# Kernel optimization log

Hardware: AMD Instinct MI355X
Metric: run time of the kernel (lower is better)

## Reference

```python
import jax, jax.numpy as jnp
import numpy as np

NEG_SLOPE = 0.2


def gat_layer(x, src, dst, W, a_src, a_dst, b, heads, out_c, concat):
    N = x.shape[0]
    h = (x @ W).reshape(N, heads, out_c)                      # [N,H,C]
    alpha_s = jnp.einsum('nhc,hc->nh', h, a_src)              # [N,H]
    alpha_d = jnp.einsum('nhc,hc->nh', h, a_dst)              # [N,H]
    e = jax.nn.leaky_relu(alpha_s[src] + alpha_d[dst], NEG_SLOPE)  # [E,H]
    # softmax over incoming edges per destination node (segment softmax)
    m = jax.ops.segment_max(e, dst, num_segments=N)
    m = jnp.where(jnp.isfinite(m), m, 0.0)
    ex = jnp.exp(e - m[dst])
    denom = jax.ops.segment_sum(ex, dst, num_segments=N)
    alpha = ex / (denom[dst] + 1e-16)                         # [E,H]
    out = jax.ops.segment_sum(alpha[:, :, None] * h[src], dst, num_segments=N)  # [N,H,C]
    out = out.reshape(N, heads * out_c) if concat else out.mean(axis=1)
    return out + b


def setup_inputs() -> dict:
    key = jax.random.key(0)
    ks = jax.random.split(key, 12)
    N, E, D, H, C, G = 20000, 160000, 256, 4, 128, 64
    x = jax.random.normal(ks[0], (N, D), dtype=jnp.float32)
    edge_index = jax.random.randint(ks[1], (2, E), 0, N)
    batch = jnp.sort(jax.random.randint(ks[2], (N,), 0, G))
    s = 0.05
    params = {
        'W1': jax.random.normal(ks[3], (D, H * C), jnp.float32) * s,
        'a_src1': jax.random.normal(ks[4], (H, C), jnp.float32) * s,
        'a_dst1': jax.random.normal(ks[5], (H, C), jnp.float32) * s,
        'b1': jnp.zeros((H * C,), jnp.float32),
        'W2': jax.random.normal(ks[6], (H * C, C), jnp.float32) * s,
        'a_src2': jax.random.normal(ks[7], (1, C), jnp.float32) * s,
        'a_dst2': jax.random.normal(ks[8], (1, C), jnp.float32) * s,
        'b2': jnp.zeros((C,), jnp.float32),
        'fc1_W': jax.random.normal(ks[9], (C, C // 2), jnp.float32) * s,
        'fc1_b': jnp.zeros((C // 2,), jnp.float32),
        'fc2_W': jax.random.normal(ks[10], (C // 2, 1), jnp.float32) * s,
        'fc2_b': jnp.zeros((1,), jnp.float32),
    }
    return dict(x=x, edge_index=edge_index, batch=batch, **params)


def reference(x, edge_index, batch, W1, a_src1, a_dst1, b1, W2, a_src2, a_dst2, b2,
              fc1_W, fc1_b, fc2_W, fc2_b):
    N = x.shape[0]
    G = 64  # number of graphs
    # add self-loops (PyG GATConv default)
    loop = jnp.arange(N, dtype=edge_index.dtype)
    src = jnp.concatenate([edge_index[0], loop])
    dst = jnp.concatenate([edge_index[1], loop])
    h = jax.nn.relu(gat_layer(x, src, dst, W1, a_src1, a_dst1, b1, 4, 128, True))
    h = gat_layer(h, src, dst, W2, a_src2, a_dst2, b2, 1, 128, False)
    # global mean pool per graph
    sums = jax.ops.segment_sum(h, batch, num_segments=G)
    cnts = jax.ops.segment_sum(jnp.ones((N,), h.dtype), batch, num_segments=G)
    pooled = sums / jnp.maximum(cnts, 1.0)[:, None]          # [G,128]
    out = jax.nn.relu(pooled @ fc1_W + fc1_b)
    return out @ fc2_W + fc2_b                                # [G,1]
```

## Files before the change

### kernel.cpp

```cpp
#include <hip/hip_runtime.h>
#include <hip/hip_bf16.h>
#include <cstdint>
#include <cstddef>

#define NEG_SLOPE 0.2f

typedef __attribute__((ext_vector_type(8))) __bf16 bf16x8;
typedef __attribute__((ext_vector_type(4))) __bf16 bf16x4;
typedef __attribute__((ext_vector_type(2))) __bf16 bf16x2;
typedef __attribute__((ext_vector_type(4))) float  f32x4;

template<int MF, int NF, bool STORE_BF16>
__global__ __launch_bounds__(256) void gemm_mfma(
    const __bf16* __restrict__ A, const __bf16* __restrict__ Bhi,
    const __bf16* __restrict__ Blo, void* __restrict__ Cout,
    int M, int N, int K)
{
    const int tid  = threadIdx.x;
    const int wave = tid >> 6, lane = tid & 63;
    const int wr = wave >> 1, wc = wave & 1;
    const int rowbase = blockIdx.y * (32 * MF) + wr * (16 * MF);
    const int colbase = blockIdx.x * (32 * NF) + wc * (16 * NF);
    const int l15 = lane & 15, kg = lane >> 4;

    size_t aoff[MF], boff[NF];
    #pragma unroll
    for (int mf = 0; mf < MF; ++mf) {
        int r = rowbase + mf * 16 + l15;
        if (r > M - 1) r = M - 1;
        aoff[mf] = (size_t)r * K + kg * 8;
    }
    #pragma unroll
    for (int nf = 0; nf < NF; ++nf) {
        int c = colbase + nf * 16 + l15;
        boff[nf] = (size_t)c * K + kg * 8;
    }

    f32x4 acc[MF][NF];
    #pragma unroll
    for (int mf = 0; mf < MF; ++mf)
        #pragma unroll
        for (int nf = 0; nf < NF; ++nf)
            acc[mf][nf] = (f32x4){0.f, 0.f, 0.f, 0.f};

    #pragma unroll 2
    for (int k0 = 0; k0 < K; k0 += 32) {
        bf16x8 af[MF], bh[NF], bl[NF];
        #pragma unroll
        for (int mf = 0; mf < MF; ++mf)
            af[mf] = *(const bf16x8*)(A + aoff[mf] + k0);
        #pragma unroll
        for (int nf = 0; nf < NF; ++nf) {
            bh[nf] = *(const bf16x8*)(Bhi + boff[nf] + k0);
            bl[nf] = *(const bf16x8*)(Blo + boff[nf] + k0);
        }
        #pragma unroll
        for (int mf = 0; mf < MF; ++mf)
            #pragma unroll
            for (int nf = 0; nf < NF; ++nf) {
                acc[mf][nf] = __builtin_amdgcn_mfma_f32_16x16x32_bf16(af[mf], bh[nf], acc[mf][nf], 0, 0, 0);
                acc[mf][nf] = __builtin_amdgcn_mfma_f32_16x16x32_bf16(af[mf], bl[nf], acc[mf][nf], 0, 0, 0);
            }
    }

    #pragma unroll
    for (int mf = 0; mf < MF; ++mf)
        #pragma unroll
        for (int j = 0; j < 4; ++j) {
            int r = rowbase + mf * 16 + kg * 4 + j;
            if (r < M) {
                #pragma unroll
                for (int nf = 0; nf < NF; ++nf) {
                    int c = colbase + nf * 16 + l15;
                    if (STORE_BF16)
                        ((__bf16*)Cout)[(size_t)r * N + c] = (__bf16)acc[mf][nf][j];
                    else
                        ((float*)Cout)[(size_t)r * N + c] = acc[mf][nf][j];
                }
            }
        }
}

__global__ void prep_kernel(const float* __restrict__ W1, const float* __restrict__ W2,
                            const float* __restrict__ as1w, const float* __restrict__ ad1w,
                            const float* __restrict__ as2w, const float* __restrict__ ad2w,
                            const int* __restrict__ batch,
                            __bf16* __restrict__ w1thi, __bf16* __restrict__ w1tlo,
                            __bf16* __restrict__ w2thi, __bf16* __restrict__ w2tlo,
                            float* __restrict__ wsd1, float* __restrict__ wsd2,
                            int* __restrict__ gstart, int* __restrict__ cnt,
                            int N, int G)
{
    int t = blockIdx.x * 256 + threadIdx.x;
    if (t < 131072) {
        int i = t;
        int k = i >> 9, n = i & 511;
        float w = W1[i];
        __bf16 hi = (__bf16)w;
        __bf16 lo = (__bf16)(w - (float)hi);
        w1thi[n * 256 + k] = hi;
        w1tlo[n * 256 + k] = lo;
    } else if (t < 196608) {
        int j = t - 131072;
        int k = j >> 7, n = j & 127;
        float w = W2[j];
        __bf16 hi = (__bf16)w;
        __bf16 lo = (__bf16)(w - (float)hi);
        w2thi[n * 512 + k] = hi;
        w2tlo[n * 512 + k] = lo;
    } else if (t < 199680) {
        int t2 = t - 196608;
        if (t2 < 2048) {
            int k = t2 >> 3, v = t2 & 7, h = v >> 1;
            const float* av = (v & 1) ? (ad1w + h * 128) : (as1w + h * 128);
            float s = 0.f;
            for (int c = 0; c < 128; ++c) s += W1[k * 512 + h * 128 + c] * av[c];
            wsd1[v * 256 + k] = s;
        } else {
            int t3 = t2 - 2048;
            int k = t3 >> 1, v = t3 & 1;
            const float* av = v ? ad2w : as2w;
            float s = 0.f;
            for (int c = 0; c < 128; ++c) s += W2[k * 128 + c] * av[c];
            wsd2[v * 512 + k] = s;
        }
    } else if (t < 199680 + N) {
        int n = t - 199680;
        int b    = batch[n];
        int prev = (n == 0) ? -1 : batch[n - 1];
        for (int g = prev + 1; g <= b; ++g) gstart[g] = n;
        if (n == N - 1) {
            for (int g = b + 1; g <= G; ++g) gstart[g] = N;
        }
    } else if (t < 199680 + 2 * N) {
        cnt[t - 199680 - N] = 0;
    }
}

__global__ __launch_bounds__(256) void cvtx_kernel(
    const float* __restrict__ x, const float* __restrict__ wsd1,
    __bf16* __restrict__ xb, float* __restrict__ as1_, float* __restrict__ ad1_, int N)
{
    int wave = threadIdx.x >> 6, lane = threadIdx.x & 63;
    int n = blockIdx.x * 4 + wave;
    if (n >= N) return;
    float4 xv = *(const float4*)&x[(size_t)n * 256 + lane * 4];
    bf16x4 xo;
    xo[0] = (__bf16)xv.x; xo[1] = (__bf16)xv.y; xo[2] = (__bf16)xv.z; xo[3] = (__bf16)xv.w;
    *(bf16x4*)&xb[(size_t)n * 256 + lane * 4] = xo;
    float p[8];
    #pragma unroll
    for (int v = 0; v < 8; ++v) {
        float4 wv = *(const float4*)&wsd1[v * 256 + lane * 4];
        p[v] = xv.x * wv.x + xv.y * wv.y + xv.z * wv.z + xv.w * wv.w;
    }
    #pragma unroll
    for (int v = 0; v < 8; ++v)
        #pragma unroll
        for (int s = 1; s < 64; s <<= 1) p[v] += __shfl_xor(p[v], s);
    if (lane == 0) {
        #pragma unroll
        for (int h = 0; h < 4; ++h) {
            as1_[n * 4 + h] = p[2 * h];
            ad1_[n * 4 + h] = p[2 * h + 1];
        }
    }
}

__global__ void count_kernel(const int* __restrict__ ei, int* __restrict__ cnt,
                             int ET, int E0)
{
    int e = blockIdx.x * blockDim.x + threadIdx.x;
    if (e >= ET) return;
    int d = (e < E0) ? ei[E0 + e] : (e - E0);
    atomicAdd(&cnt[d], 1);
}

__global__ void scan1(const int* __restrict__ cnt, int* __restrict__ offs,
                      int* __restrict__ bsum, int n)
{
    __shared__ int tmp[256];
    int t = threadIdx.x;
    int i = blockIdx.x * 256 + t;
    int v = (i < n) ? cnt[i] : 0;
    tmp[t] = v;
    __syncthreads();
    for (int s = 1; s < 256; s <<= 1) {
        int a = (t >= s) ? tmp[t - s] : 0;
        __syncthreads();
        tmp[t] += a;
        __syncthreads();
    }
    if (i < n) offs[i] = tmp[t] - v;
    if (t == 255) bsum[blockIdx.x] = tmp[255];
}

__global__ void scan2(const int* __restrict__ bsum, int* __restrict__ bofs,
                      int B, int* __restrict__ total_dst)
{
    __shared__ int tmp[256];
    int t = threadIdx.x;
    int v = (t < B) ? bsum[t] : 0;
    tmp[t] = v;
    __syncthreads();
    for (int s = 1; s < 256; s <<= 1) {
        int a = (t >= s) ? tmp[t - s] : 0;
        __syncthreads();
        tmp[t] += a;
        __syncthreads();
    }
    if (t < B) bofs[t] = tmp[t] - v;
    if (t == 255) *total_dst = tmp[255];
}

__global__ void scan3(int* __restrict__ offs, const int* __restrict__ bofs,
                      int* __restrict__ cur, int n)
{
    int i = blockIdx.x * 256 + threadIdx.x;
    if (i < n) {
        int o = offs[i] + bofs[blockIdx.x];
        offs[i] = o;
        cur[i]  = o;
    }
}

__global__ void scatter_kernel(const int* __restrict__ ei, int* __restrict__ cur,
                               int* __restrict__ eid, int ET, int E0)
{
    int e = blockIdx.x * blockDim.x + threadIdx.x;
    if (e >= ET) return;
    int d   = (e < E0) ? ei[E0 + e] : (e - E0);
    int pos = atomicAdd(&cur[d], 1);
    eid[pos] = e;
}

__global__ __launch_bounds__(256) void aggregate1_kernel(
    const __bf16* __restrict__ h1b, const int* __restrict__ offs,
    const int* __restrict__ eid, const int* __restrict__ ei,
    const float* __restrict__ as1_, const float* __restrict__ ad1_,
    const float* __restrict__ b1, const float* __restrict__ wsd2,
    __bf16* __restrict__ out1b, float* __restrict__ as2_, float* __restrict__ ad2_,
    int E0, int N)
{
    int wave = threadIdx.x >> 6, lane = threadIdx.x & 63;
    int n = blockIdx.x * 4 + wave;
    if (n >= N) return;
    int hd  = lane >> 4;
    int l16 = lane & 15;
    int s0 = offs[n], s1 = offs[n + 1];
    float adn = ad1_[n * 4 + hd];

    float m = -1e30f;
    for (int j = s0 + l16; j < s1; j += 16) {
        int e = eid[j];
        int s = (e < E0) ? ei[e] : (e - E0);
        float v = as1_[s * 4 + hd] + adn;
        v = (v < 0.f) ? NEG_SLOPE * v : v;
        m = fmaxf(m, v);
    }
    #pragma unroll
    for (int t = 1; t < 16; t <<= 1) m = fmaxf(m, __shfl_xor(m, t));
    float den = 0.f;
    for (int j = s0 + l16; j < s1; j += 16) {
        int e = eid[j];
        int s = (e < E0) ? ei[e] : (e - E0);
        float v = as1_[s * 4 + hd] + adn;
        v = (v < 0.f) ? NEG_SLOPE * v : v;
        den += __expf(v - m);
    }
    #pragma unroll
    for (int t = 1; t < 16; t <<= 1) den += __shfl_xor(den, t);
    float inv = 1.f / (den + 1e-16f);

    float a[8] = {0.f, 0.f, 0.f, 0.f, 0.f, 0.f, 0.f, 0.f};
    const __bf16* hbase = h1b + lane * 8;
    int j = s0;
    for (; j + 3 < s1; j += 4) {
        int e0 = eid[j], e1 = eid[j + 1], e2 = eid[j + 2], e3 = eid[j + 3];
        int sA = (e0 < E0) ? ei[e0] : (e0 - E0);
        int sB = (e1 < E0) ? ei[e1] : (e1 - E0);
        int sC = (e2 < E0) ? ei[e2] : (e2 - E0);
        int sD = (e3 < E0) ? ei[e3] : (e3 - E0);
        float vA = as1_[sA * 4 + hd] + adn;
        float vB = as1_[sB * 4 + hd] + adn;
        float vC = as1_[sC * 4 + hd] + adn;
        float vD = as1_[sD * 4 + hd] + adn;
        bf16x8 hA = *(const bf16x8*)(hbase + (size_t)sA * 512);
        bf16x8 hB = *(const bf16x8*)(hbase + (size_t)sB * 512);
        bf16x8 hC = *(const bf16x8*)(hbase + (size_t)sC * 512);
        bf16x8 hD = *(const bf16x8*)(hbase + (size_t)sD * 512);
        vA = (vA < 0.f) ? NEG_SLOPE * vA : vA;
        vB = (vB < 0.f) ? NEG_SLOPE * vB : vB;
        vC = (vC < 0.f) ? NEG_SLOPE * vC : vC;
        vD = (vD < 0.f) ? NEG_SLOPE * vD : vD;
        float wA = __expf(vA - m) * inv;
        float wB = __expf(vB - m) * inv;
        float wC = __expf(vC - m) * inv;
        float wD = __expf(vD - m) * inv;
        #pragma unroll
        for (int i = 0; i < 8; ++i) {
            a[i] = fmaf(wA, (float)hA[i], a[i]);
            a[i] = fmaf(wB, (float)hB[i], a[i]);
            a[i] = fmaf(wC, (float)hC[i], a[i]);
            a[i] = fmaf(wD, (float)hD[i], a[i]);
        }
    }
    for (; j < s1; ++j) {
        int e = eid[j];
        int s = (e < E0) ? ei[e] : (e - E0);
        float v = as1_[s * 4 + hd] + adn;
        v = (v < 0.f) ? NEG_SLOPE * v : v;
        float w = __expf(v - m) * inv;
        bf16x8 hv = *(const bf16x8*)(hbase + (size_t)s * 512);
        #pragma unroll
        for (int i = 0; i < 8; ++i) a[i] = fmaf(w, (float)hv[i], a[i]);
    }

    bf16x8 ov;
    float ps = 0.f, pd = 0.f;
    #pragma unroll
    for (int i = 0; i < 8; ++i) {
        float o = fmaxf(a[i] + b1[lane * 8 + i], 0.f);
        ov[i] = (__bf16)o;
        ps = fmaf(o, wsd2[lane * 8 + i], ps);
        pd = fmaf(o, wsd2[512 + lane * 8 + i], pd);
    }
    *(bf16x8*)&out1b[(size_t)n * 512 + lane * 8] = ov;
    #pragma unroll
    for (int t = 1; t < 64; t <<= 1) {
        ps += __shfl_xor(ps, t);
        pd += __shfl_xor(pd, t);
    }
    if (lane == 0) {
        as2_[n] = ps;
        ad2_[n] = pd;
    }
}

__global__ __launch_bounds__(256) void aggregate2_kernel(
    const __bf16* __restrict__ h2b, const int* __restrict__ offs,
    const int* __restrict__ eid, const int* __restrict__ ei,
    const float* __restrict__ as2_, const float* __restrict__ ad2_,
    const float* __restrict__ b2, float* __restrict__ out2, int E0, int N)
{
    int wave = threadIdx.x >> 6, lane = threadIdx.x & 63;
    int n = blockIdx.x * 4 + wave;
    if (n >= N) return;
    int s0 = offs[n], s1 = offs[n + 1];
    float adn = ad2_[n];

    float m = -1e30f;
    for (int j = s0 + lane; j < s1; j += 64) {
        int e = eid[j];
        int s = (e < E0) ? ei[e] : (e - E0);
        float v = as2_[s] + adn;
        v = (v < 0.f) ? NEG_SLOPE * v : v;
        m = fmaxf(m, v);
    }
    #pragma unroll
    for (int t = 1; t < 64; t <<= 1) m = fmaxf(m, __shfl_xor(m, t));
    float den = 0.f;
    for (int j = s0 + lane; j < s1; j += 64) {
        int e = eid[j];
        int s = (e < E0) ? ei[e] : (e - E0);
        float v = as2_[s] + adn;
        v = (v < 0.f) ? NEG_SLOPE * v : v;
        den += __expf(v - m);
    }
    #pragma unroll
    for (int t = 1; t < 64; t <<= 1) den += __shfl_xor(den, t);
    float inv = 1.f / (den + 1e-16f);

    float a0 = 0.f, a1 = 0.f;
    const __bf16* hbase = h2b + lane * 2;
    int j = s0;
    for (; j + 3 < s1; j += 4) {
        int e0 = eid[j], e1 = eid[j + 1], e2 = eid[j + 2], e3 = eid[j + 3];
        int sA = (e0 < E0) ? ei[e0] : (e0 - E0);
        int sB = (e1 < E0) ? ei[e1] : (e1 - E0);
        int sC = (e2 < E0) ? ei[e2] : (e2 - E0);
        int sD = (e3 < E0) ? ei[e3] : (e3 - E0);
        float vA = as2_[sA] + adn;
        float vB = as2_[sB] + adn;
        float vC = as2_[sC] + adn;
        float vD = as2_[sD] + adn;
        bf16x2 hA = *(const bf16x2*)(hbase + (size_t)sA * 128);
        bf16x2 hB = *(const bf16x2*)(hbase + (size_t)sB * 128);
        bf16x2 hC = *(const bf16x2*)(hbase + (size_t)sC * 128);
        bf16x2 hD = *(const bf16x2*)(hbase + (size_t)sD * 128);
        vA = (vA < 0.f) ? NEG_SLOPE * vA : vA;
        vB = (vB < 0.f) ? NEG_SLOPE * vB : vB;
        vC = (vC < 0.f) ? NEG_SLOPE * vC : vC;
        vD = (vD < 0.f) ? NEG_SLOPE * vD : vD;
        float wA = __expf(vA - m) * inv;
        float wB = __expf(vB - m) * inv;
        float wC = __expf(vC - m) * inv;
        float wD = __expf(vD - m) * inv;
        a0 = fmaf(wA, (float)hA[0], a0); a1 = fmaf(wA, (float)hA[1], a1);
        a0 = fmaf(wB, (float)hB[0], a0); a1 = fmaf(wB, (float)hB[1], a1);
        a0 = fmaf(wC, (float)hC[0], a0); a1 = fmaf(wC, (float)hC[1], a1);
        a0 = fmaf(wD, (float)hD[0], a0); a1 = fmaf(wD, (float)hD[1], a1);
    }
    for (; j < s1; ++j) {
        int e = eid[j];
        int s = (e < E0) ? ei[e] : (e - E0);
        float v = as2_[s] + adn;
        v = (v < 0.f) ? NEG_SLOPE * v : v;
        float w = __expf(v - m) * inv;
        bf16x2 hv = *(const bf16x2*)(hbase + (size_t)s * 128);
        a0 = fmaf(w, (float)hv[0], a0);
        a1 = fmaf(w, (float)hv[1], a1);
    }
    float2 o;
    o.x = a0 + b2[lane * 2 + 0];
    o.y = a1 + b2[lane * 2 + 1];
    *(float2*)&out2[(size_t)n * 128 + lane * 2] = o;
}

#define POOL_S 16
__global__ void pool_stage1(const float* __restrict__ out2, const int* __restrict__ gstart,
                            float* __restrict__ partial, int C)
{
    int g = blockIdx.x, slice = blockIdx.y;
    int c = threadIdx.x;
    int s = gstart[g], e = gstart[g + 1];
    int len = e - s;
    int chunk = (len + POOL_S - 1) / POOL_S;
    int n0 = s + slice * chunk;
    int n1 = min(n0 + chunk, e);
    float acc = 0.f;
    for (int n = n0; n < n1; ++n) acc += out2[(size_t)n * C + c];
    partial[((size_t)g * POOL_S + slice) * C + c] = acc;
}

__global__ void pool_stage2(const float* __restrict__ partial, const int* __restrict__ gstart,
                            float* __restrict__ pooled, int C)
{
    int g = blockIdx.x;
    int c = threadIdx.x;
    float acc = 0.f;
    #pragma unroll
    for (int s = 0; s < POOL_S; ++s)
        acc += partial[((size_t)g * POOL_S + s) * C + c];
    float cntf = (float)(gstart[g + 1] - gstart[g]);
    pooled[(size_t)g * C + c] = acc / fmaxf(cntf, 1.0f);
}

__global__ void head_kernel(const float* __restrict__ pooled, const float* __restrict__ fc1W,
                            const float* __restrict__ fc1b, const float* __restrict__ fc2W,
                            const float* __restrict__ fc2b, float* __restrict__ out)
{
    int g = blockIdx.x;
    int j = threadIdx.x;
    float t = 0.f;
    for (int c = 0; c < 128; ++c)
        t += pooled[(size_t)g * 128 + c] * fc1W[c * 64 + j];
    t = fmaxf(t + fc1b[j], 0.f);
    float v = t * fc2W[j];
    #pragma unroll
    for (int s = 32; s > 0; s >>= 1) v += __shfl_down(v, s);
    if (j == 0) out[g] = v + fc2b[0];
}

extern "C" void kernel_launch(void* const* d_in, const int* in_sizes, int n_in,
                              void* d_out, int out_size, void* d_ws, size_t ws_size,
                              hipStream_t stream)
{
    const float* x    = (const float*)d_in[0];
    const int*   ei   = (const int*)d_in[1];
    const int*   batch= (const int*)d_in[2];
    const float* W1   = (const float*)d_in[3];
    const float* as1w = (const float*)d_in[4];
    const float* ad1w = (const float*)d_in[5];
    const float* b1   = (const float*)d_in[6];
    const float* W2   = (const float*)d_in[7];
    const float* as2w = (const float*)d_in[8];
    const float* ad2w = (const float*)d_in[9];
    const float* b2   = (const float*)d_in[10];
    const float* fc1W = (const float*)d_in[11];
    const float* fc1b = (const float*)d_in[12];
    const float* fc2W = (const float*)d_in[13];
    const float* fc2b = (const float*)d_in[14];
    float* out = (float*)d_out;

    const int D = 256, C = 128, HC = 512, G = 64;
    const int N  = in_sizes[0] / D;
    const int E0 = in_sizes[1] / 2;
    const int ET = E0 + N;
    const int NB = (N + 255) / 256;

    char* p = (char*)d_ws;
    auto alloc = [&](size_t bytes) -> char* {
        char* r = p;
        p += (bytes + 255) & ~(size_t)255;
        return r;
    };
    __bf16* xb    = (__bf16*)alloc((size_t)N * D * 2);
    __bf16* h1b   = (__bf16*)alloc((size_t)N * HC * 2);
    __bf16* out1b = (__bf16*)alloc((size_t)N * HC * 2);
    __bf16* h2b   = (__bf16*)alloc((size_t)N * C * 2);
    float*  out2  = (float*)alloc((size_t)N * C * 4);
    __bf16* w1thi = (__bf16*)alloc((size_t)256 * 512 * 2);
    __bf16* w1tlo = (__bf16*)alloc((size_t)256 * 512 * 2);
    __bf16* w2thi = (__bf16*)alloc((size_t)512 * 128 * 2);
    __bf16* w2tlo = (__bf16*)alloc((size_t)512 * 128 * 2);
    float* wsd1 = (float*)alloc(8 * 256 * 4);
    float* wsd2 = (float*)alloc(2 * 512 * 4);
    float* as1_ = (float*)alloc((size_t)N * 4 * 4);
    float* ad1_ = (float*)alloc((size_t)N * 4 * 4);
    float* as2_ = (float*)alloc((size_t)N * 4);
    float* ad2_ = (float*)alloc((size_t)N * 4);
    int*   cnt    = (int*)alloc((size_t)N * 4);
    int*   cur    = (int*)alloc((size_t)N * 4);
    int*   offs   = (int*)alloc((size_t)(N + 1) * 4);
    int*   eid    = (int*)alloc((size_t)ET * 4);
    int*   bsum   = (int*)alloc(256 * 4);
    int*   bofs   = (int*)alloc(256 * 4);
    int*   gstart = (int*)alloc((size_t)(G + 1) * 4);
    float* partial= (float*)alloc((size_t)G * POOL_S * C * 4);
    float* pooled = (float*)alloc((size_t)G * C * 4);

    {
        int total = 199680 + 2 * N;
        prep_kernel<<<(total + 255) / 256, 256, 0, stream>>>(
            W1, W2, as1w, ad1w, as2w, ad2w, batch,
            w1thi, w1tlo, w2thi, w2tlo, wsd1, wsd2, gstart, cnt, N, G);
    }

    count_kernel<<<(ET + 255) / 256, 256, 0, stream>>>(ei, cnt, ET, E0);
    scan1<<<NB, 256, 0, stream>>>(cnt, offs, bsum, N);
    scan2<<<1, 256, 0, stream>>>(bsum, bofs, NB, offs + N);
    scan3<<<NB, 256, 0, stream>>>(offs, bofs, cur, N);
    scatter_kernel<<<(ET + 255) / 256, 256, 0, stream>>>(ei, cur, eid, ET, E0);

    cvtx_kernel<<<N / 4, 256, 0, stream>>>(x, wsd1, xb, as1_, ad1_, N);

    gemm_mfma<4, 4, true><<<dim3(HC / 128, (N + 127) / 128), 256, 0, stream>>>(
        xb, w1thi, w1tlo, h1b, N, HC, D);
    aggregate1_kernel<<<(N + 3) / 4, 256, 0, stream>>>(
        h1b, offs, eid, ei, as1_, ad1_, b1, wsd2, out1b, as2_, ad2_, E0, N);

    gemm_mfma<2, 2, true><<<dim3(C / 64, (N + 63) / 64), 256, 0, stream>>>(
        out1b, w2thi, w2tlo, h2b, N, C, HC);
    aggregate2_kernel<<<(N + 3) / 4, 256, 0, stream>>>(
        h2b, offs, eid, ei, as2_, ad2_, b2, out2, E0, N);

    pool_stage1<<<dim3(G, POOL_S), C, 0, stream>>>(out2, gstart, partial, C);
    pool_stage2<<<G, C, 0, stream>>>(partial, gstart, pooled, C);
    head_kernel<<<G, 64, 0, stream>>>(pooled, fc1W, fc1b, fc2W, fc2b, out);
}
```

Baseline: 201.5 us.

## Drop split-bf16 weights, fuse scan and pool/head, single-pass softmax aggregation

Drops the hi/lo bf16 split of W1/W2, so each GEMM issues half as many MFMAs and B-loads, at some cost in accuracy. The three-kernel prefix scan becomes one 1024-thread block scan, and pool_stage2 and the head are fused into one kernel. Both aggregation kernels now accumulate the softmax denominator in the same pass as the weighted sum and normalize once at the end, removing a second gather pass over edges. The gather loop is also unrolled by 8 for more memory-level parallelism. The single-block scan has CHUNK hardcoded at 20, which only covers N up to 20480.

Result: faster. 196.7 us (-2.4%).

```diff
diff --git a/kernel.cpp b/kernel.cpp
--- a/kernel.cpp
+++ b/kernel.cpp
@@ -12,9 +12,8 @@
 
 template<int MF, int NF, bool STORE_BF16>
 __global__ __launch_bounds__(256) void gemm_mfma(
-    const __bf16* __restrict__ A, const __bf16* __restrict__ Bhi,
-    const __bf16* __restrict__ Blo, void* __restrict__ Cout,
-    int M, int N, int K)
+    const __bf16* __restrict__ A, const __bf16* __restrict__ Bt,
+    void* __restrict__ Cout, int M, int N, int K)
 {
     const int tid  = threadIdx.x;
     const int wave = tid >> 6, lane = tid & 63;
@@ -45,22 +44,18 @@
 
     #pragma unroll 2
     for (int k0 = 0; k0 < K; k0 += 32) {
-        bf16x8 af[MF], bh[NF], bl[NF];
+        bf16x8 af[MF], bf[NF];
         #pragma unroll
         for (int mf = 0; mf < MF; ++mf)
             af[mf] = *(const bf16x8*)(A + aoff[mf] + k0);
         #pragma unroll
-        for (int nf = 0; nf < NF; ++nf) {
-            bh[nf] = *(const bf16x8*)(Bhi + boff[nf] + k0);
-            bl[nf] = *(const bf16x8*)(Blo + boff[nf] + k0);
-        }
+        for (int nf = 0; nf < NF; ++nf)
+            bf[nf] = *(const bf16x8*)(Bt + boff[nf] + k0);
         #pragma unroll
         for (int mf = 0; mf < MF; ++mf)
             #pragma unroll
-            for (int nf = 0; nf < NF; ++nf) {
-                acc[mf][nf] = __builtin_amdgcn_mfma_f32_16x16x32_bf16(af[mf], bh[nf], acc[mf][nf], 0, 0, 0);
-                acc[mf][nf] = __builtin_amdgcn_mfma_f32_16x16x32_bf16(af[mf], bl[nf], acc[mf][nf], 0, 0, 0);
-            }
+            for (int nf = 0; nf < NF; ++nf)
+                acc[mf][nf] = __builtin_amdgcn_mfma_f32_16x16x32_bf16(af[mf], bf[nf], acc[mf][nf], 0, 0, 0);
     }
 
     #pragma unroll
@@ -85,8 +80,7 @@
                             const float* __restrict__ as1w, const float* __restrict__ ad1w,
                             const float* __restrict__ as2w, const float* __restrict__ ad2w,
                             const int* __restrict__ batch,
-                            __bf16* __restrict__ w1thi, __bf16* __restrict__ w1tlo,
-                            __bf16* __restrict__ w2thi, __bf16* __restrict__ w2tlo,
+                            __bf16* __restrict__ w1t, __bf16* __restrict__ w2t,
                             float* __restrict__ wsd1, float* __restrict__ wsd2,
                             int* __restrict__ gstart, int* __restrict__ cnt,
                             int N, int G)
@@ -95,19 +89,11 @@
     if (t < 131072) {
         int i = t;
         int k = i >> 9, n = i & 511;
-        float w = W1[i];
-        __bf16 hi = (__bf16)w;
-        __bf16 lo = (__bf16)(w - (float)hi);
-        w1thi[n * 256 + k] = hi;
-        w1tlo[n * 256 + k] = lo;
+        w1t[n * 256 + k] = (__bf16)W1[i];
     } else if (t < 196608) {
         int j = t - 131072;
         int k = j >> 7, n = j & 127;
-        float w = W2[j];
-        __bf16 hi = (__bf16)w;
-        __bf16 lo = (__bf16)(w - (float)hi);
-        w2thi[n * 512 + k] = hi;
-        w2tlo[n * 512 + k] = lo;
+        w2t[n * 512 + k] = (__bf16)W2[j];
     } else if (t < 199680) {
         int t2 = t - 196608;
         if (t2 < 2048) {
@@ -176,52 +162,47 @@
     atomicAdd(&cnt[d], 1);
 }
 
-__global__ void scan1(const int* __restrict__ cnt, int* __restrict__ offs,
-                      int* __restrict__ bsum, int n)
-{
-    __shared__ int tmp[256];
+__global__ __launch_bounds__(1024) void scan_fused(
+    const int* __restrict__ cnt, int* __restrict__ offs, int* __restrict__ cur, int n)
+{
+    constexpr int CHUNK = 20;
     int t = threadIdx.x;
-    int i = blockIdx.x * 256 + t;
-    int v = (i < n) ? cnt[i] : 0;
-    tmp[t] = v;
+    int base = t * CHUNK;
+    int v[CHUNK];
+    int s = 0;
+    #pragma unroll
+    for (int i = 0; i < CHUNK; ++i) {
+        int idx = base + i;
+        int xv = (idx < n) ? cnt[idx] : 0;
+        v[i] = s; s += xv;
+    }
+    int lane = t & 63, w = t >> 6;
+    int sc = s;
+    #pragma unroll
+    for (int d = 1; d < 64; d <<= 1) {
+        int o = __shfl_up(sc, d);
+        if (lane >= d) sc += o;
+    }
+    __shared__ int wt[16], wb[17];
+    if (lane == 63) wt[w] = sc;
     __syncthreads();
-    for (int s = 1; s < 256; s <<= 1) {
-        int a = (t >= s) ? tmp[t - s] : 0;
-        __syncthreads();
-        tmp[t] += a;
-        __syncthreads();
-    }
-    if (i < n) offs[i] = tmp[t] - v;
-    if (t == 255) bsum[blockIdx.x] = tmp[255];
-}
-
-__global__ void scan2(const int* __restrict__ bsum, int* __restrict__ bofs,
-                      int B, int* __restrict__ total_dst)
-{
-    __shared__ int tmp[256];
-    int t = threadIdx.x;
-    int v = (t < B) ? bsum[t] : 0;
-    tmp[t] = v;
+    if (t == 0) {
+        int acc = 0;
+        for (int i = 0; i < 16; ++i) { wb[i] = acc; acc += wt[i]; }
+        wb[16] = acc;
+    }
     __syncthreads();
-    for (int s = 1; s < 256; s <<= 1) {
-        int a = (t >= s) ? tmp[t - s] : 0;
-        __syncthreads();
-        tmp[t] += a;
-        __syncthreads();
-    }
-    if (t < B) bofs[t] = tmp[t] - v;
-    if (t == 255) *total_dst = tmp[255];
-}
-
-__global__ void scan3(int* __restrict__ offs, const int* __restrict__ bofs,
-                      int* __restrict__ cur, int n)
-{
-    int i = blockIdx.x * 256 + threadIdx.x;
-    if (i < n) {
-        int o = offs[i] + bofs[blockIdx.x];
-        offs[i] = o;
-        cur[i]  = o;
-    }
+    int ebase = wb[w] + (sc - s);
+    #pragma unroll
+    for (int i = 0; i < CHUNK; ++i) {
+        int idx = base + i;
+        if (idx < n) {
+            int o = ebase + v[i];
+            offs[idx] = o;
+            cur[idx]  = o;
+        }
+    }
+    if (t == 0) offs[n] = wb[16];
 }
 
 __global__ void scatter_kernel(const int* __restrict__ ei, int* __restrict__ cur,
@@ -260,49 +241,31 @@
     }
     #pragma unroll
     for (int t = 1; t < 16; t <<= 1) m = fmaxf(m, __shfl_xor(m, t));
+
     float den = 0.f;
-    for (int j = s0 + l16; j < s1; j += 16) {
-        int e = eid[j];
-        int s = (e < E0) ? ei[e] : (e - E0);
-        float v = as1_[s * 4 + hd] + adn;
-        v = (v < 0.f) ? NEG_SLOPE * v : v;
-        den += __expf(v - m);
-    }
-    #pragma unroll
-    for (int t = 1; t < 16; t <<= 1) den += __shfl_xor(den, t);
-    float inv = 1.f / (den + 1e-16f);
-
     float a[8] = {0.f, 0.f, 0.f, 0.f, 0.f, 0.f, 0.f, 0.f};
     const __bf16* hbase = h1b + lane * 8;
     int j = s0;
-    for (; j + 3 < s1; j += 4) {
-        int e0 = eid[j], e1 = eid[j + 1], e2 = eid[j + 2], e3 = eid[j + 3];
-        int sA = (e0 < E0) ? ei[e0] : (e0 - E0);
-        int sB = (e1 < E0) ? ei[e1] : (e1 - E0);
-        int sC = (e2 < E0) ? ei[e2] : (e2 - E0);
-        int sD = (e3 < E0) ? ei[e3] : (e3 - E0);
-        float vA = as1_[sA * 4 + hd] + adn;
-        float vB = as1_[sB * 4 + hd] + adn;
-        float vC = as1_[sC * 4 + hd] + adn;
-        float vD = as1_[sD * 4 + hd] + adn;
-        bf16x8 hA = *(const bf16x8*)(hbase + (size_t)sA * 512);
-        bf16x8 hB = *(const bf16x8*)(hbase + (size_t)sB * 512);
-        bf16x8 hC = *(const bf16x8*)(hbase + (size_t)sC * 512);
-        bf16x8 hD = *(const bf16x8*)(hbase + (size_t)sD * 512);
-        vA = (vA < 0.f) ? NEG_SLOPE * vA : vA;
-        vB = (vB < 0.f) ? NEG_SLOPE * vB : vB;
-        vC = (vC < 0.f) ? NEG_SLOPE * vC : vC;
-        vD = (vD < 0.f) ? NEG_SLOPE * vD : vD;
-        float wA = __expf(vA - m) * inv;
-        float wB = __expf(vB - m) * inv;
-        float wC = __expf(vC - m) * inv;
-        float wD = __expf(vD - m) * inv;
+    for (; j + 7 < s1; j += 8) {
+        int e_[8], s_[8];
+        float v_[8];
+        bf16x8 h_[8];
+        #pragma unroll
+        for (int i = 0; i < 8; ++i) e_[i] = eid[j + i];
+        #pragma unroll
+        for (int i = 0; i < 8; ++i) s_[i] = (e_[i] < E0) ? ei[e_[i]] : (e_[i] - E0);
+        #pragma unroll
+        for (int i = 0; i < 8; ++i) v_[i] = as1_[s_[i] * 4 + hd] + adn;
+        #pragma unroll
+        for (int i = 0; i < 8; ++i) h_[i] = *(const bf16x8*)(hbase + (size_t)s_[i] * 512);
         #pragma unroll
         for (int i = 0; i < 8; ++i) {
-            a[i] = fmaf(wA, (float)hA[i], a[i]);
-            a[i] = fmaf(wB, (float)hB[i], a[i]);
-            a[i] = fmaf(wC, (float)hC[i], a[i]);
-            a[i] = fmaf(wD, (float)hD[i], a[i]);
+            float v = (v_[i] < 0.f) ? NEG_SLOPE * v_[i] : v_[i];
+            float w = __expf(v - m);
+            den += w;
+            #pragma unroll
+            for (int k = 0; k < 8; ++k)
+                a[k] = fmaf(w, (float)h_[i][k], a[k]);
         }
     }
     for (; j < s1; ++j) {
@@ -310,17 +273,19 @@
         int s = (e < E0) ? ei[e] : (e - E0);
         float v = as1_[s * 4 + hd] + adn;
         v = (v < 0.f) ? NEG_SLOPE * v : v;
-        float w = __expf(v - m) * inv;
+        float w = __expf(v - m);
+        den += w;
         bf16x8 hv = *(const bf16x8*)(hbase + (size_t)s * 512);
         #pragma unroll
-        for (int i = 0; i < 8; ++i) a[i] = fmaf(w, (float)hv[i], a[i]);
-    }
+        for (int k = 0; k < 8; ++k) a[k] = fmaf(w, (float)hv[k], a[k]);
+    }
+    float inv = 1.f / (den + 1e-16f);
 
     bf16x8 ov;
     float ps = 0.f, pd = 0.f;
     #pragma unroll
     for (int i = 0; i < 8; ++i) {
-        float o = fmaxf(a[i] + b1[lane * 8 + i], 0.f);
+        float o = fmaxf(a[i] * inv + b1[lane * 8 + i], 0.f);
         ov[i] = (__bf16)o;
         ps = fmaf(o, wsd2[lane * 8 + i], ps);
         pd = fmaf(o, wsd2[512 + lane * 8 + i], pd);
@@ -359,61 +324,47 @@
     }
     #pragma unroll
     for (int t = 1; t < 64; t <<= 1) m = fmaxf(m, __shfl_xor(m, t));
+
     float den = 0.f;
-    for (int j = s0 + lane; j < s1; j += 64) {
-        int e = eid[j];
-        int s = (e < E0) ? ei[e] : (e - E0);
-        float v = as2_[s] + adn;
-        v = (v < 0.f) ? NEG_SLOPE * v : v;
-        den += __expf(v - m);
-    }
-    #pragma unroll
-    for (int t = 1; t < 64; t <<= 1) den += __shfl_xor(den, t);
-    float inv = 1.f / (den + 1e-16f);
-
     float a0 = 0.f, a1 = 0.f;
     const __bf16* hbase = h2b + lane * 2;
     int j = s0;
-    for (; j + 3 < s1; j += 4) {
-        int e0 = eid[j], e1 = eid[j + 1], e2 = eid[j + 2], e3 = eid[j + 3];
-        int sA = (e0 < E0) ? ei[e0] : (e0 - E0);
-        int sB = (e1 < E0) ? ei[e1] : (e1 - E0);
-        int sC = (e2 < E0) ? ei[e2] : (e2 - E0);
-        int sD = (e3 < E0) ? ei[e3] : (e3 - E0);
-        float vA = as2_[sA] + adn;
-        float vB = as2_[sB] + adn;
-        float vC = as2_[sC] + adn;
-        float vD = as2_[sD] + adn;
-        bf16x2 hA = *(const bf16x2*)(hbase + (size_t)sA * 128);
-        bf16x2 hB = *(const bf16x2*)(hbase + (size_t)sB * 128);
-        bf16x2 hC = *(const bf16x2*)(hbase + (size_t)sC * 128);
-        bf16x2 hD = *(const bf16x2*)(hbase + (size_t)sD * 128);
-        vA = (vA < 0.f) ? NEG_SLOPE * vA : vA;
-        vB = (vB < 0.f) ? NEG_SLOPE * vB : vB;
-        vC = (vC < 0.f) ? NEG_SLOPE * vC : vC;
-        vD = (vD < 0.f) ? NEG_SLOPE * vD : vD;
-        float wA = __expf(vA - m) * inv;
-        float wB = __expf(vB - m) * inv;
-        float wC = __expf(vC - m) * inv;
-        float wD = __expf(vD - m) * inv;
-        a0 = fmaf(wA, (float)hA[0], a0); a1 = fmaf(wA, (float)hA[1], a1);
-        a0 = fmaf(wB, (float)hB[0], a0); a1 = fmaf(wB, (float)hB[1], a1);
-        a0 = fmaf(wC, (float)hC[0], a0); a1 = fmaf(wC, (float)hC[1], a1);
-        a0 = fmaf(wD, (float)hD[0], a0); a1 = fmaf(wD, (float)hD[1], a1);
+    for (; j + 7 < s1; j += 8) {
+        int e_[8], s_[8];
+        float v_[8];
+        bf16x2 h_[8];
+        #pragma unroll
+        for (int i = 0; i < 8; ++i) e_[i] = eid[j + i];
+        #pragma unroll
+        for (int i = 0; i < 8; ++i) s_[i] = (e_[i] < E0) ? ei[e_[i]] : (e_[i] - E0);
+        #pragma unroll
+        for (int i = 0; i < 8; ++i) v_[i] = as2_[s_[i]] + adn;
+        #pragma unroll
+        for (int i = 0; i < 8; ++i) h_[i] = *(const bf16x2*)(hbase + (size_t)s_[i] * 128);
+        #pragma unroll
+        for (int i = 0; i < 8; ++i) {
+            float v = (v_[i] < 0.f) ? NEG_SLOPE * v_[i] : v_[i];
+            float w = __expf(v - m);
+            den += w;
+            a0 = fmaf(w, (float)h_[i][0], a0);
+            a1 = fmaf(w, (float)h_[i][1], a1);
+        }
     }
     for (; j < s1; ++j) {
         int e = eid[j];
         int s = (e < E0) ? ei[e] : (e - E0);
         float v = as2_[s] + adn;
         v = (v < 0.f) ? NEG_SLOPE * v : v;
-        float w = __expf(v - m) * inv;
+        float w = __expf(v - m);
+        den += w;
         bf16x2 hv = *(const bf16x2*)(hbase + (size_t)s * 128);
         a0 = fmaf(w, (float)hv[0], a0);
         a1 = fmaf(w, (float)hv[1], a1);
     }
+    float inv = 1.f / (den + 1e-16f);
     float2 o;
-    o.x = a0 + b2[lane * 2 + 0];
-    o.y = a1 + b2[lane * 2 + 1];
+    o.x = a0 * inv + b2[lane * 2 + 0];
+    o.y = a1 * inv + b2[lane * 2 + 1];
     *(float2*)&out2[(size_t)n * 128 + lane * 2] = o;
 }
 
@@ -433,33 +384,31 @@
     partial[((size_t)g * POOL_S + slice) * C + c] = acc;
 }
 
-__global__ void pool_stage2(const float* __restrict__ partial, const int* __restrict__ gstart,
-                            float* __restrict__ pooled, int C)
+__global__ __launch_bounds__(128) void pool_head(
+    const float* __restrict__ partial, const int* __restrict__ gstart,
+    const float* __restrict__ fc1W, const float* __restrict__ fc1b,
+    const float* __restrict__ fc2W, const float* __restrict__ fc2b,
+    float* __restrict__ out)
 {
     int g = blockIdx.x;
-    int c = threadIdx.x;
+    int t = threadIdx.x;
+    __shared__ float pl[128];
     float acc = 0.f;
     #pragma unroll
     for (int s = 0; s < POOL_S; ++s)
-        acc += partial[((size_t)g * POOL_S + s) * C + c];
+        acc += partial[((size_t)g * POOL_S + s) * 128 + t];
     float cntf = (float)(gstart[g + 1] - gstart[g]);
-    pooled[(size_t)g * C + c] = acc / fmaxf(cntf, 1.0f);
-}
-
-__global__ void head_kernel(const float* __restrict__ pooled, const float* __restrict__ fc1W,
-                            const float* __restrict__ fc1b, const float* __restrict__ fc2W,
-                            const float* __restrict__ fc2b, float* __restrict__ out)
-{
-    int g = blockIdx.x;
-    int j = threadIdx.x;
-    float t = 0.f;
-    for (int c = 0; c < 128; ++c)
-        t += pooled[(size_t)g * 128 + c] * fc1W[c * 64 + j];
-    t = fmaxf(t + fc1b[j], 0.f);
-    float v = t * fc2W[j];
-    #pragma unroll
-    for (int s = 32; s > 0; s >>= 1) v += __shfl_down(v, s);
-    if (j == 0) out[g] = v + fc2b[0];
+    pl[t] = acc / fmaxf(cntf, 1.0f);
+    __syncthreads();
+    if (t < 64) {
+        float v = 0.f;
+        for (int c = 0; c < 128; ++c)
+            v += pl[c] * fc1W[c * 64 + t];
+        v = fmaxf(v + fc1b[t], 0.f) * fc2W[t];
+        #pragma unroll
+        for (int s = 32; s > 0; s >>= 1) v += __shfl_down(v, s);
+        if (t == 0) out[g] = v + fc2b[0];
+    }
 }
 
 extern "C" void kernel_launch(void* const* d_in, const int* in_sizes, int n_in,
@@ -487,7 +436,6 @@
     const int N  = in_sizes[0] / D;
     const int E0 = in_sizes[1] / 2;
     const int ET = E0 + N;
-    const int NB = (N + 255) / 256;
 
     char* p = (char*)d_ws;
     auto alloc = [&](size_t bytes) -> char* {
@@ -500,10 +448,8 @@
     __bf16* out1b = (__bf16*)alloc((size_t)N * HC * 2);
     __bf16* h2b   = (__bf16*)alloc((size_t)N * C * 2);
     float*  out2  = (float*)alloc((size_t)N * C * 4);
-    __bf16* w1thi = (__bf16*)alloc((size_t)256 * 512 * 2);
-    __bf16* w1tlo = (__bf16*)alloc((size_t)256 * 512 * 2);
-    __bf16* w2thi = (__bf16*)alloc((size_t)512 * 128 * 2);
-    __bf16* w2tlo = (__bf16*)alloc((size_t)512 * 128 * 2);
+    __bf16* w1t   = (__bf16*)alloc((size_t)256 * 512 * 2);
+    __bf16* w2t   = (__bf16*)alloc((size_t)512 * 128 * 2);
     float* wsd1 = (float*)alloc(8 * 256 * 4);
     float* wsd2 = (float*)alloc(2 * 512 * 4);
     float* as1_ = (float*)alloc((size_t)N * 4 * 4);
@@ -514,38 +460,32 @@
     int*   cur    = (int*)alloc((size_t)N * 4);
     int*   offs   = (int*)alloc((size_t)(N + 1) * 4);
     int*   eid    = (int*)alloc((size_t)ET * 4);
-    int*   bsum   = (int*)alloc(256 * 4);
-    int*   bofs   = (int*)alloc(256 * 4);
     int*   gstart = (int*)alloc((size_t)(G + 1) * 4);
     float* partial= (float*)alloc((size_t)G * POOL_S * C * 4);
-    float* pooled = (float*)alloc((size_t)G * C * 4);
 
     {
         int total = 199680 + 2 * N;
         prep_kernel<<<(total + 255) / 256, 256, 0, stream>>>(
             W1, W2, as1w, ad1w, as2w, ad2w, batch,
-            w1thi, w1tlo, w2thi, w2tlo, wsd1, wsd2, gstart, cnt, N, G);
+            w1t, w2t, wsd1, wsd2, gstart, cnt, N, G);
     }
 
     count_kernel<<<(ET + 255) / 256, 256, 0, stream>>>(ei, cnt, ET, E0);
-    scan1<<<NB, 256, 0, stream>>>(cnt, offs, bsum, N);
-    scan2<<<1, 256, 0, stream>>>(bsum, bofs, NB, offs + N);
-    scan3<<<NB, 256, 0, stream>>>(offs, bofs, cur, N);
+    scan_fused<<<1, 1024, 0, stream>>>(cnt, offs, cur, N);
     scatter_kernel<<<(ET + 255) / 256, 256, 0, stream>>>(ei, cur, eid, ET, E0);
 
     cvtx_kernel<<<N / 4, 256, 0, stream>>>(x, wsd1, xb, as1_, ad1_, N);
 
     gemm_mfma<4, 4, true><<<dim3(HC / 128, (N + 127) / 128), 256, 0, stream>>>(
-        xb, w1thi, w1tlo, h1b, N, HC, D);
+        xb, w1t, h1b, N, HC, D);
     aggregate1_kernel<<<(N + 3) / 4, 256, 0, stream>>>(
         h1b, offs, eid, ei, as1_, ad1_, b1, wsd2, out1b, as2_, ad2_, E0, N);
 
     gemm_mfma<2, 2, true><<<dim3(C / 64, (N + 63) / 64), 256, 0, stream>>>(
-        out1b, w2thi, w2tlo, h2b, N, C, HC);
+        out1b, w2t, h2b, N, C, HC);
     aggregate2_kernel<<<(N + 3) / 4, 256, 0, stream>>>(
         h2b, offs, eid, ei, as2_, ad2_, b2, out2, E0, N);
 
     pool_stage1<<<dim3(G, POOL_S), C, 0, stream>>>(out2, gstart, partial, C);
-    pool_stage2<<<G, C, 0, stream>>>(partial, gstart, pooled, C);
-    head_kernel<<<G, 64, 0, stream>>>(pooled, fc1W, fc1b, fc2W, fc2b, out);
-}
+    pool_head<<<G, 128, 0, stream>>>(partial, gstart, fc1W, fc1b, fc2W, fc2b, out);
+}
```
